# Performance work log

Hardware: AMD Instinct MI355X
Metric: run time of the kernel (lower is better)

## Reference

```python
import jax, jax.numpy as jnp
import numpy as np

K, N, D, M, M_RF, N_RF = 512, 512, 16, 64, 16, 64


def cmul(a, b):
    # complex matmul with stacked real/imag in axis -3: a [...,2,m,k], b [...,2,k,n]
    ar, ai = a[..., 0, :, :], a[..., 1, :, :]
    br, bi = b[..., 0, :, :], b[..., 1, :, :]
    return jnp.stack([ar @ br - ai @ bi, ar @ bi + ai @ br], axis=-3)


def conjT(a):
    # complex conjugate transpose
    ar, ai = a[..., 0, :, :], a[..., 1, :, :]
    return jnp.stack([jnp.swapaxes(ar, -1, -2), -jnp.swapaxes(ai, -1, -2)], axis=-3)


def cinv(a):
    # inverse of complex matrix a=[2,n,n] via real 2n x 2n block matrix
    ar, ai = a[0], a[1]
    n = ar.shape[0]
    Mblk = jnp.block([[ar, -ai], [ai, ar]])
    Minv = jnp.linalg.inv(Mblk)
    return jnp.stack([Minv[:n, :n], Minv[n:, :n]], axis=0)


def setup_inputs() -> dict:
    key = jax.random.key(0)
    ks = jax.random.split(key, 8)
    s = 0.05  # keep accumulated products well-scaled
    H = s * jax.random.normal(ks[0], (K, 2, M, N), jnp.float32)
    U_RF = s * jax.random.normal(ks[1], (K, 2, M, M_RF), jnp.float32)
    U_BB = s * jax.random.normal(ks[2], (K, 2, M_RF, D), jnp.float32)
    W = s * jax.random.normal(ks[3], (K, 2, D, D), jnp.float32)
    V_RF = s * jax.random.normal(ks[4], (2, N, N_RF), jnp.float32)
    V_BB = s * jax.random.normal(ks[5], (K, 2, N_RF, D), jnp.float32)
    Y = s * jax.random.normal(ks[6], (K, 2, N, D), jnp.float32)
    rho = jnp.ones((1,), jnp.float32)  # forward arg, unused by the module
    rho_X_layer = jnp.asarray(6.0, jnp.float32)  # learned scalar
    mu = jnp.asarray(1.0, jnp.float32)           # learned scalar
    params4 = 0.001 * jax.random.normal(ks[7], (K, 2, N, D), jnp.float32)
    return dict(H=H, U_RF=U_RF, U_BB=U_BB, W=W, V_RF=V_RF, V_BB=V_BB, Y=Y,
                rho=rho, rho_X_layer=rho_X_layer, mu=mu, params4=params4)


def reference(H, U_RF, U_BB, W, V_RF, V_BB, Y, rho, rho_X_layer, mu, params4):
    # temp[k] = H[k]^H U_RF[k] U_BB[k] : [K,2,N,d]
    temp = cmul(cmul(conjT(H), U_RF), U_BB)
    TW = cmul(temp, W)  # [K,2,N,d]
    # A_rho = sum_k temp W temp^H + I/(2 rho) : [2,N,N]
    A_rho = cmul(TW, conjT(temp)).sum(axis=0)
    I = jnp.stack([jnp.eye(N, dtype=H.dtype), jnp.zeros((N, N), H.dtype)], axis=0)
    A_rho = A_rho + (1.0 / (2.0 * rho_X_layer)) * I
    # B_rho[k] = temp W + 0.5*(V_RF V_BB[k]/rho - Y[k]) : [K,2,N,d]
    B_rho = TW + 0.5 * ((1.0 / rho_X_layer) * cmul(V_RF, V_BB) - Y)
    A_inv = cinv(A_rho + mu * I)  # [2,N,N]
    X = cmul(A_inv, B_rho) + params4  # [K,2,N,d]
    return X
```

## Files before the change

### kernel.cpp

```cpp
#include <hip/hip_runtime.h>

#define KK 512
#define NN 512
#define DD 16
#define MM 64
#define MRF 16
#define NRF 64

typedef __attribute__((ext_vector_type(8))) short bf16x8;
typedef __attribute__((ext_vector_type(4))) float f32x4;
typedef __attribute__((ext_vector_type(8))) unsigned short u16x8;
typedef __attribute__((ext_vector_type(4))) unsigned short u16x4;

#define MFMA16 __builtin_amdgcn_mfma_f32_16x16x32_bf16

static __device__ __forceinline__ unsigned short f2bf(float x) {
    unsigned int u = __float_as_uint(x);
    u += 0x7fffu + ((u >> 16) & 1u);
    return (unsigned short)(u >> 16);
}
static __device__ __forceinline__ float bf2f(unsigned short b) {
    return __uint_as_float((unsigned int)b << 16);
}
static __device__ __forceinline__ unsigned int pk2(float lo, float hi) {
    return (unsigned int)f2bf(lo) | ((unsigned int)f2bf(hi) << 16);
}

union frag_cast { uint4 u; bf16x8 v; };

__global__ __launch_bounds__(256) void vrfb_kernel(
    const float* __restrict__ V_RF, unsigned short* __restrict__ VRFb)
{
    const int idx = blockIdx.x*256 + threadIdx.x;
    const int n = idx >> 7, j = idx & 127;
    const int p = j >> 6, r = j & 63;
    VRFb[idx] = f2bf(V_RF[((size_t)p*NN + n)*NRF + r]);
}

__global__ __launch_bounds__(256) void small_kernel(
    const float* __restrict__ U_RF, const float* __restrict__ U_BB,
    const float* __restrict__ W, const float* __restrict__ V_BB,
    unsigned int* __restrict__ GT2f)
{
    const int k = blockIdx.x, t = threadIdx.x;
    __shared__ float sUR[2][MM][17];
    __shared__ float sUB[2][MRF][DD], sW[2][DD][DD];
    __shared__ float sVB[2][NRF][17];
    __shared__ float sG[2][MM][17], sGW[2][MM][17];

    const float* uf = U_RF + (size_t)k*2*MM*MRF;
    for (int i = t; i < 2*MM*MRF; i += 256) sUR[i>>10][(i>>4)&63][i&15] = uf[i];
    const float* ub = U_BB + (size_t)k*2*MRF*DD;
    for (int i = t; i < 2*MRF*DD; i += 256) sUB[i>>8][(i>>4)&15][i&15] = ub[i];
    const float* ww = W + (size_t)k*2*DD*DD;
    for (int i = t; i < 2*DD*DD; i += 256) sW[i>>8][(i>>4)&15][i&15] = ww[i];
    const float* vb = V_BB + (size_t)k*2*NRF*DD;
    for (int i = t; i < 2*NRF*DD; i += 256) sVB[i>>10][(i>>4)&63][i&15] = vb[i];
    __syncthreads();

    {
        const int m = t >> 2, dq = (t & 3) * 4;
        float gr[4] = {0,0,0,0}, gi[4] = {0,0,0,0};
#pragma unroll
        for (int r = 0; r < MRF; ++r) {
            const float ur = sUR[0][m][r], ui = sUR[1][m][r];
#pragma unroll
            for (int q = 0; q < 4; ++q) {
                const float br = sUB[0][r][dq+q], bi = sUB[1][r][dq+q];
                gr[q] += ur*br - ui*bi;
                gi[q] += ur*bi + ui*br;
            }
        }
#pragma unroll
        for (int q = 0; q < 4; ++q) { sG[0][m][dq+q] = gr[q]; sG[1][m][dq+q] = gi[q]; }
    }
    __syncthreads();

    {
        const int m = t >> 2, dq = (t & 3) * 4;
        float gwr[4] = {0,0,0,0}, gwi[4] = {0,0,0,0};
#pragma unroll
        for (int dp = 0; dp < DD; ++dp) {
            const float gr = sG[0][m][dp], gi = sG[1][m][dp];
#pragma unroll
            for (int q = 0; q < 4; ++q) {
                const float wr = sW[0][dp][dq+q], wi = sW[1][dp][dq+q];
                gwr[q] += gr*wr - gi*wi;
                gwi[q] += gr*wi + gi*wr;
            }
        }
#pragma unroll
        for (int q = 0; q < 4; ++q) { sGW[0][m][dq+q] = gwr[q]; sGW[1][m][dq+q] = gwi[q]; }
    }
    __syncthreads();

    {
        const int lane64 = t & 63, ks = t >> 6;
        const int c = lane64 & 15, kg = lane64 >> 4;
        const int e2b = ks*16 + kg*4;
        unsigned int* dstk = GT2f + (size_t)k*6144 + ks*1536 + lane64*4;
#pragma unroll
        for (int s = 0; s < 6; ++s) {
            uint4 o;
#pragma unroll
            for (int j = 0; j < 4; ++j) {
                const int e2 = e2b + j;
                const int sl0 = 2*e2;
                const int m0 = sl0 & 63, hi = sl0 >> 6;
                const int m1 = m0 + 1;
                float v0, v1;
                if (s == 0)      { v0 = hi ? sG[1][m0][c]   : sG[0][m0][c];
                                   v1 = hi ? sG[1][m1][c]   : sG[0][m1][c]; }
                else if (s == 1) { v0 = hi ? -sG[0][m0][c]  : sG[1][m0][c];
                                   v1 = hi ? -sG[0][m1][c]  : sG[1][m1][c]; }
                else if (s == 2) { v0 = hi ? sGW[1][m0][c]  : sGW[0][m0][c];
                                   v1 = hi ? sGW[1][m1][c]  : sGW[0][m1][c]; }
                else if (s == 3) { v0 = hi ? -sGW[0][m0][c] : sGW[1][m0][c];
                                   v1 = hi ? -sGW[0][m1][c] : sGW[1][m1][c]; }
                else if (s == 4) { v0 = hi ? -sVB[1][m0][c] : sVB[0][m0][c];
                                   v1 = hi ? -sVB[1][m1][c] : sVB[0][m1][c]; }
                else             { v0 = hi ? sVB[0][m0][c]  : sVB[1][m0][c];
                                   v1 = hi ? sVB[0][m1][c]  : sVB[1][m1][c]; }
                ((unsigned int*)&o)[j] = pk2(v0, v1);
            }
            *reinterpret_cast<uint4*>(dstk + s*256) = o;
        }
    }
}

__global__ __launch_bounds__(512, 8) void prep_main(
    const float* __restrict__ H, const unsigned int* __restrict__ GT2f,
    const unsigned short* __restrict__ VRFb,
    const float* __restrict__ Y, const float* __restrict__ rhoX,
    unsigned short* __restrict__ tempb, unsigned short* __restrict__ TWb,
    unsigned short* __restrict__ Bb)
{
    const int nb = blockIdx.x & 3;
    const int k  = blockIdx.x >> 2;
    const int t  = threadIdx.x;
    const int n0 = nb*128;

    __shared__ unsigned int sH[64][129];

    const float* Hk = H + (size_t)k*128*NN + n0;
#pragma unroll
    for (int pass = 0; pass < 4; ++pass) {
        const int e2 = pass*16 + (t >> 5);
        const int c4 = (t & 31) * 4;
        const float4 a = *reinterpret_cast<const float4*>(Hk + (size_t)(2*e2  )*NN + c4);
        const float4 b = *reinterpret_cast<const float4*>(Hk + (size_t)(2*e2+1)*NN + c4);
        uint4 d;
        d.x = pk2(a.x, b.x); d.y = pk2(a.y, b.y);
        d.z = pk2(a.z, b.z); d.w = pk2(a.w, b.w);
        *reinterpret_cast<uint4*>(&sH[e2][c4]) = d;
    }

    const int w = t >> 6, lane = t & 63;
    const int c = lane & 15, kg = lane >> 4;
    const float irx = 1.f / rhoX[0];
    const int ncol = w*16 + c;
    const int n = n0 + ncol;

    const size_t o0 = ((size_t)(k*2 + 0)*NN + n)*DD + kg*4;
    const size_t o1 = ((size_t)(k*2 + 1)*NN + n)*DD + kg*4;
    const float4 y0 = *reinterpret_cast<const float4*>(Y + o0);
    const float4 y1 = *reinterpret_cast<const float4*>(Y + o1);

    __syncthreads();

    f32x4 aTr = (f32x4)0.f, aTi = (f32x4)0.f;
    f32x4 aWr = (f32x4)0.f, aWi = (f32x4)0.f;
    f32x4 aVr = (f32x4)0.f, aVi = (f32x4)0.f;

    const unsigned int* gk = GT2f + (size_t)k*6144 + lane*4;

#pragma unroll
    for (int ks = 0; ks < 4; ++ks) {
        const int slot0 = ks*32 + kg*8;
        const int e2b = ks*16 + kg*4;
        frag_cast fh, g0, g1, g2, g3, v0, v1;
        fh.u.x = sH[e2b+0][ncol];
        fh.u.y = sH[e2b+1][ncol];
        fh.u.z = sH[e2b+2][ncol];
        fh.u.w = sH[e2b+3][ncol];
        const unsigned int* gb = gk + ks*1536;
        g0.u = *reinterpret_cast<const uint4*>(gb);
        g1.u = *reinterpret_cast<const uint4*>(gb + 256);
        g2.u = *reinterpret_cast<const uint4*>(gb + 512);
        g3.u = *reinterpret_cast<const uint4*>(gb + 768);
        v0.u = *reinterpret_cast<const uint4*>(gb + 1024);
        v1.u = *reinterpret_cast<const uint4*>(gb + 1280);
        const bf16x8 bv = *reinterpret_cast<const bf16x8*>(VRFb + (size_t)n*128 + slot0);

        aTr = MFMA16(g0.v, fh.v, aTr, 0, 0, 0);
        aTi = MFMA16(g1.v, fh.v, aTi, 0, 0, 0);
        aWr = MFMA16(g2.v, fh.v, aWr, 0, 0, 0);
        aWi = MFMA16(g3.v, fh.v, aWi, 0, 0, 0);
        aVr = MFMA16(v0.v, bv, aVr, 0, 0, 0);
        aVi = MFMA16(v1.v, bv, aVi, 0, 0, 0);
    }

    {
        const float y0a[4] = {y0.x, y0.y, y0.z, y0.w};
        const float y1a[4] = {y1.x, y1.y, y1.z, y1.w};
        u16x4 tr_, ti_, wr_, wi_, br_, bi_;
#pragma unroll
        for (int r = 0; r < 4; ++r) {
            tr_[r] = f2bf(aTr[r]);  ti_[r] = f2bf(aTi[r]);
            wr_[r] = f2bf(aWr[r]);  wi_[r] = f2bf(aWi[r]);
            br_[r] = f2bf(aWr[r] + 0.5f*(aVr[r]*irx - y0a[r]));
            bi_[r] = f2bf(aWi[r] + 0.5f*(aVi[r]*irx - y1a[r]));
        }
        *reinterpret_cast<u16x4*>(tempb + o0) = tr_;
        *reinterpret_cast<u16x4*>(tempb + o1) = ti_;
        *reinterpret_cast<u16x4*>(TWb + o0)   = wr_;
        *reinterpret_cast<u16x4*>(TWb + o1)   = wi_;
        *reinterpret_cast<u16x4*>(Bb + o0)    = br_;
        *reinterpret_cast<u16x4*>(Bb + o1)    = bi_;
    }
}

__global__ __launch_bounds__(256) void egemm_kernel(
    const unsigned short* __restrict__ TWb, const unsigned short* __restrict__ tmpb,
    float* __restrict__ Epart)
{
    const int ib = blockIdx.x >> 3;
    const int ks = blockIdx.x & 7;
    const int jb = blockIdx.y;
    const int w    = threadIdx.x >> 6;
    const int lane = threadIdx.x & 63;
    const int m  = lane & 15;
    const int kg = lane >> 4;
    const int iw = ib*64 + (w>>1)*32;
    const int jw = jb*64 + (w&1)*32;
    const int d0  = (kg & 1) * 8;
    const int kof = kg >> 1;

    f32x4 RR[2][2], II[2][2], RI[2][2], IR[2][2];
#pragma unroll
    for (int is = 0; is < 2; ++is)
#pragma unroll
        for (int js = 0; js < 2; ++js) {
            RR[is][js] = (f32x4)0.f; II[is][js] = (f32x4)0.f;
            RI[is][js] = (f32x4)0.f; IR[is][js] = (f32x4)0.f;
        }

#pragma unroll 2
    for (int c = 0; c < 32; ++c) {
        const int chunk = ks*32 + c;
        const int kp = chunk*2 + kof;
        const unsigned short* Ab = TWb  + ((size_t)(kp*2+0)*NN + iw + m)*DD + d0;
        const unsigned short* Bb2 = tmpb + ((size_t)(kp*2+0)*NN + jw + m)*DD + d0;
        bf16x8 ar[2], ai[2], br[2], bi[2];
#pragma unroll
        for (int is = 0; is < 2; ++is) {
            ar[is] = *reinterpret_cast<const bf16x8*>(Ab + (size_t)is*16*DD);
            ai[is] = *reinterpret_cast<const bf16x8*>(Ab + (size_t)NN*DD + (size_t)is*16*DD);
        }
#pragma unroll
        for (int js = 0; js < 2; ++js) {
            br[js] = *reinterpret_cast<const bf16x8*>(Bb2 + (size_t)js*16*DD);
            bi[js] = *reinterpret_cast<const bf16x8*>(Bb2 + (size_t)NN*DD + (size_t)js*16*DD);
        }
#pragma unroll
        for (int is = 0; is < 2; ++is)
#pragma unroll
            for (int js = 0; js < 2; ++js) {
                RR[is][js] = MFMA16(ar[is], br[js], RR[is][js], 0, 0, 0);
                II[is][js] = MFMA16(ai[is], bi[js], II[is][js], 0, 0, 0);
                RI[is][js] = MFMA16(ar[is], bi[js], RI[is][js], 0, 0, 0);
                IR[is][js] = MFMA16(ai[is], br[js], IR[is][js], 0, 0, 0);
            }
    }

    float* Eb = Epart + (size_t)ks*2*NN*NN;
#pragma unroll
    for (int is = 0; is < 2; ++is)
#pragma unroll
        for (int js = 0; js < 2; ++js) {
            const int i = iw + is*16 + kg*4;
            const int jx = jw + js*16 + m;
#pragma unroll
            for (int r = 0; r < 4; ++r) {
                Eb[(size_t)(i+r)*NN + jx]               = RR[is][js][r] + II[is][js][r];
                Eb[(size_t)NN*NN + (size_t)(i+r)*NN + jx] = IR[is][js][r] - RI[is][js][r];
            }
        }
}

__global__ __launch_bounds__(256) void reduceinit_kernel(
    const float* __restrict__ Epart,
    const float* __restrict__ rhoX, const float* __restrict__ mu,
    unsigned short* __restrict__ P, unsigned short* __restrict__ PT,
    unsigned short* __restrict__ T1, unsigned short* __restrict__ T1T)
{
    const size_t idx = (size_t)blockIdx.x*256 + threadIdx.x;
    const float ic = 1.f / (1.f/(2.f*rhoX[0]) + mu[0]);
    const size_t pl = (size_t)2*NN*NN;
    float s = 0.f;
#pragma unroll
    for (int ks = 0; ks < 8; ++ks) s += Epart[(size_t)ks*pl + idx];
    const float mm = s * ic;
    const int p = (int)(idx / ((size_t)NN*NN));
    const size_t rem = idx - (size_t)p*NN*NN;
    const int i = (int)(rem / NN), jx = (int)(rem % NN);
    const unsigned short pv = f2bf(-mm);
    const unsigned short tv = f2bf(((p == 0 && i == jx) ? 1.f : 0.f) - mm);
    const size_t tidx = (size_t)p*NN*NN + (size_t)jx*NN + i;
    P[idx] = pv;  PT[tidx] = pv;
    T1[idx] = tv; T1T[tidx] = tv;
}

template<bool ADD_B, bool WRITE_T>
__global__ __launch_bounds__(256) void mm_kernel(
    const unsigned short* __restrict__ A, const unsigned short* __restrict__ BT,
    unsigned short* __restrict__ D, unsigned short* __restrict__ DT)
{
    const int w    = threadIdx.x >> 6;
    const int lane = threadIdx.x & 63;
    const int m  = lane & 15;
    const int kg = lane >> 4;
    const int i0 = blockIdx.y*32;
    const int j0 = blockIdx.x*32;
    const int iw = (w>>1)*16;
    const int jw = (w&1)*16;

    __shared__ unsigned short sD[2][32][34];

    f32x4 RR = (f32x4)0.f, II = (f32x4)0.f, RI = (f32x4)0.f, IR = (f32x4)0.f;

#pragma unroll 8
    for (int c = 0; c < 16; ++c) {
        const int l0 = c*32 + kg*8;
        const bf16x8 ar = *reinterpret_cast<const bf16x8*>(A  + (size_t)(i0+iw+m)*NN + l0);
        const bf16x8 ai = *reinterpret_cast<const bf16x8*>(A  + (size_t)NN*NN + (size_t)(i0+iw+m)*NN + l0);
        const bf16x8 br = *reinterpret_cast<const bf16x8*>(BT + (size_t)(j0+jw+m)*NN + l0);
        const bf16x8 bi = *reinterpret_cast<const bf16x8*>(BT + (size_t)NN*NN + (size_t)(j0+jw+m)*NN + l0);
        RR = MFMA16(ar, br, RR, 0, 0, 0);
        II = MFMA16(ai, bi, II, 0, 0, 0);
        RI = MFMA16(ar, bi, RI, 0, 0, 0);
        IR = MFMA16(ai, br, IR, 0, 0, 0);
    }
    const int i = i0 + iw + kg*4;
    const int jx = j0 + jw + m;
    float adr[4] = {0.f,0.f,0.f,0.f}, adi[4] = {0.f,0.f,0.f,0.f};
    if (ADD_B) {
        const u16x4 badr = *reinterpret_cast<const u16x4*>(BT + (size_t)jx*NN + i);
        const u16x4 badi = *reinterpret_cast<const u16x4*>(BT + (size_t)NN*NN + (size_t)jx*NN + i);
#pragma unroll
        for (int r = 0; r < 4; ++r) { adr[r] = bf2f(badr[r]); adi[r] = bf2f(badi[r]); }
    }
#pragma unroll
    for (int r = 0; r < 4; ++r) {
        const unsigned short dr_ = f2bf(RR[r] - II[r] + adr[r]);
        const unsigned short di_ = f2bf(RI[r] + IR[r] + adi[r]);
        D[(size_t)(i+r)*NN + jx] = dr_;
        D[(size_t)NN*NN + (size_t)(i+r)*NN + jx] = di_;
        if (WRITE_T) {
            sD[0][iw + kg*4 + r][jw + m] = dr_;
            sD[1][iw + kg*4 + r][jw + m] = di_;
        }
    }
    if (WRITE_T) {
        __syncthreads();
        const int t = threadIdx.x;
        const int r8 = t >> 2, seg = t & 3;
        const int plane = r8 >> 5, jloc = r8 & 31;
        u16x8 v;
#pragma unroll
        for (int e = 0; e < 8; ++e) v[e] = sD[plane][seg*8 + e][jloc];
        *reinterpret_cast<u16x8*>(DT + (size_t)plane*NN*NN +
                                  (size_t)(j0 + jloc)*NN + i0 + seg*8) = v;
    }
}

__global__ __launch_bounds__(256) void final_kernel(
    const unsigned short* __restrict__ Sb, const unsigned short* __restrict__ Bb,
    const float* __restrict__ par4,
    const float* __restrict__ rhoX, const float* __restrict__ mu,
    float* __restrict__ Xout)
{
    const int k0 = blockIdx.x * 2;
    __shared__ __align__(16) unsigned short sBT[2][2][DD][520];

#pragma unroll
    for (int kk = 0; kk < 2; ++kk) {
        const unsigned short* Bk = Bb + (size_t)(k0 + kk)*2*NN*DD;
        for (int q = 0; q < 8; ++q) {
            const int t8 = q*256 + threadIdx.x;
            const u16x8 v = *reinterpret_cast<const u16x8*>(Bk + (size_t)t8*8);
            const int flat = t8*8;
            const int p = flat >> 13, n = (flat >> 4) & 511, dd0 = flat & 15;
#pragma unroll
            for (int jj = 0; jj < 8; ++jj) sBT[kk][p][dd0+jj][n] = v[jj];
        }
    }
    __syncthreads();

    const int w    = threadIdx.x >> 6;
    const int lane = threadIdx.x & 63;
    const int m  = lane & 15;
    const int kg = lane >> 4;
    const int i0 = blockIdx.y*64 + w*16;

    f32x4 RR[2], II[2], RI[2], IR[2];
#pragma unroll
    for (int kk = 0; kk < 2; ++kk) {
        RR[kk] = (f32x4)0.f; II[kk] = (f32x4)0.f;
        RI[kk] = (f32x4)0.f; IR[kk] = (f32x4)0.f;
    }

#pragma unroll 2
    for (int c = 0; c < 16; ++c) {
        const int l0 = c*32 + kg*8;
        const bf16x8 ar = *reinterpret_cast<const bf16x8*>(Sb + (size_t)(i0+m)*NN + l0);
        const bf16x8 ai = *reinterpret_cast<const bf16x8*>(Sb + (size_t)NN*NN + (size_t)(i0+m)*NN + l0);
#pragma unroll
        for (int kk = 0; kk < 2; ++kk) {
            const bf16x8 br = *reinterpret_cast<const bf16x8*>(&sBT[kk][0][m][l0]);
            const bf16x8 bi = *reinterpret_cast<const bf16x8*>(&sBT[kk][1][m][l0]);
            RR[kk] = MFMA16(ar, br, RR[kk], 0, 0, 0);
            II[kk] = MFMA16(ai, bi, II[kk], 0, 0, 0);
            RI[kk] = MFMA16(ar, bi, RI[kk], 0, 0, 0);
            IR[kk] = MFMA16(ai, br, IR[kk], 0, 0, 0);
        }
    }
    const float ic = 1.f / (1.f/(2.f*rhoX[0]) + mu[0]);
#pragma unroll
    for (int kk = 0; kk < 2; ++kk) {
        const int k = k0 + kk;
#pragma unroll
        for (int r = 0; r < 4; ++r) {
            const int i = i0 + kg*4 + r;
            const int d = m;
            const size_t idx0 = ((size_t)(k*2+0)*NN + i)*DD + d;
            const size_t idx1 = ((size_t)(k*2+1)*NN + i)*DD + d;
            Xout[idx0] = (RR[kk][r] - II[kk][r])*ic + par4[idx0];
            Xout[idx1] = (RI[kk][r] + IR[kk][r])*ic + par4[idx1];
        }
    }
}

extern "C" void kernel_launch(void* const* d_in, const int* in_sizes, int n_in,
                              void* d_out, int out_size, void* d_ws, size_t ws_size,
                              hipStream_t stream) {
    const float* H     = (const float*)d_in[0];
    const float* U_RF  = (const float*)d_in[1];
    const float* U_BB  = (const float*)d_in[2];
    const float* W     = (const float*)d_in[3];
    const float* V_RF  = (const float*)d_in[4];
    const float* V_BB  = (const float*)d_in[5];
    const float* Y     = (const float*)d_in[6];
    const float* rhoX  = (const float*)d_in[8];
    const float* mu    = (const float*)d_in[9];
    const float* par4  = (const float*)d_in[10];
    float* Xout = (float*)d_out;

    unsigned short* u = (unsigned short*)d_ws;
    const size_t bigE = (size_t)KK*2*NN*DD;
    const size_t plE  = (size_t)2*NN*NN;
    unsigned short* tempb = u;
    unsigned short* TWb   = tempb + bigE;
    unsigned short* Bb    = TWb + bigE;
    unsigned int*   GT2f  = (unsigned int*)(Bb + bigE);
    unsigned short* VRFb  = (unsigned short*)(GT2f + (size_t)KK*6144);
    unsigned short* Pm    = VRFb + (size_t)NN*128;
    unsigned short* PmT   = Pm  + plE;
    unsigned short* T1    = PmT + plE;
    unsigned short* T1T   = T1  + plE;
    unsigned short* Q     = T1T + plE;
    unsigned short* QT    = Q   + plE;
    unsigned short* R     = QT  + plE;
    unsigned short* RT    = R   + plE;
    unsigned short* T2    = RT  + plE;
    unsigned short* T2T   = T2  + plE;
    unsigned short* T3    = T2T + plE;
    unsigned short* T3T   = T3  + plE;
    unsigned short* R2    = T3T + plE;
    unsigned short* Ss    = R2  + plE;
    float* Epart = (float*)(Ss + plE);

    vrfb_kernel<<<256, 256, 0, stream>>>(V_RF, VRFb);
    small_kernel<<<KK, 256, 0, stream>>>(U_RF, U_BB, W, V_BB, GT2f);
    prep_main<<<KK*4, 512, 0, stream>>>(H, GT2f, VRFb, Y, rhoX,
                                        tempb, TWb, Bb);
    egemm_kernel<<<dim3(64, 8), 256, 0, stream>>>(TWb, tempb, Epart);
    reduceinit_kernel<<<(int)(plE/256), 256, 0, stream>>>(Epart, rhoX, mu,
                                                          Pm, PmT, T1, T1T);
    mm_kernel<false,true ><<<dim3(16,16), 256, 0, stream>>>(Pm, PmT, Q,  QT);
    mm_kernel<true ,true ><<<dim3(16,16), 256, 0, stream>>>(Q,  T1T, T2, T2T);
    mm_kernel<false,true ><<<dim3(16,16), 256, 0, stream>>>(Q,  QT,  R,  RT);
    mm_kernel<true ,true ><<<dim3(16,16), 256, 0, stream>>>(R,  T2T, T3, T3T);
    mm_kernel<false,false><<<dim3(16,16), 256, 0, stream>>>(R,  RT,  R2, nullptr);
    mm_kernel<true ,false><<<dim3(16,16), 256, 0, stream>>>(R2, T3T, Ss, nullptr);
    final_kernel<<<dim3(KK/2, 8), 256, 0, stream>>>(Ss, Bb, par4, rhoX, mu, Xout);
}
```

Before: 218.7 us.

## Fold V_RF conversion into small_kernel and widen prep_main tiles to 256 columns

```diff
diff --git a/kernel.cpp b/kernel.cpp
--- a/kernel.cpp
+++ b/kernel.cpp
@@ -28,25 +28,22 @@
 
 union frag_cast { uint4 u; bf16x8 v; };
 
-__global__ __launch_bounds__(256) void vrfb_kernel(
-    const float* __restrict__ V_RF, unsigned short* __restrict__ VRFb)
-{
-    const int idx = blockIdx.x*256 + threadIdx.x;
-    const int n = idx >> 7, j = idx & 127;
-    const int p = j >> 6, r = j & 63;
-    VRFb[idx] = f2bf(V_RF[((size_t)p*NN + n)*NRF + r]);
-}
-
 __global__ __launch_bounds__(256) void small_kernel(
     const float* __restrict__ U_RF, const float* __restrict__ U_BB,
     const float* __restrict__ W, const float* __restrict__ V_BB,
-    unsigned int* __restrict__ GT2f)
+    const float* __restrict__ V_RF,
+    unsigned int* __restrict__ GT2f, unsigned short* __restrict__ VRFb)
 {
     const int k = blockIdx.x, t = threadIdx.x;
     __shared__ float sUR[2][MM][17];
     __shared__ float sUB[2][MRF][DD], sW[2][DD][DD];
     __shared__ float sVB[2][NRF][17];
     __shared__ float sG[2][MM][17], sGW[2][MM][17];
+
+    if (t < 128) {
+        const int p = t >> 6, r = t & 63;
+        VRFb[(size_t)k*128 + t] = f2bf(V_RF[((size_t)p*NN + k)*NRF + r]);
+    }
 
     const float* uf = U_RF + (size_t)k*2*MM*MRF;
     for (int i = t; i < 2*MM*MRF; i += 256) sUR[i>>10][(i>>4)&63][i&15] = uf[i];
@@ -128,25 +125,25 @@
     }
 }
 
-__global__ __launch_bounds__(512, 8) void prep_main(
+__global__ __launch_bounds__(512, 4) void prep_main(
     const float* __restrict__ H, const unsigned int* __restrict__ GT2f,
     const unsigned short* __restrict__ VRFb,
     const float* __restrict__ Y, const float* __restrict__ rhoX,
     unsigned short* __restrict__ tempb, unsigned short* __restrict__ TWb,
     unsigned short* __restrict__ Bb)
 {
-    const int nb = blockIdx.x & 3;
-    const int k  = blockIdx.x >> 2;
+    const int nb = blockIdx.x & 1;
+    const int k  = blockIdx.x >> 1;
     const int t  = threadIdx.x;
-    const int n0 = nb*128;
-
-    __shared__ unsigned int sH[64][129];
+    const int n0 = nb*256;
+
+    __shared__ unsigned int sH[64][260];
 
     const float* Hk = H + (size_t)k*128*NN + n0;
 #pragma unroll
-    for (int pass = 0; pass < 4; ++pass) {
-        const int e2 = pass*16 + (t >> 5);
-        const int c4 = (t & 31) * 4;
+    for (int pass = 0; pass < 8; ++pass) {
+        const int e2 = pass*8 + (t >> 6);
+        const int c4 = (t & 63) * 4;
         const float4 a = *reinterpret_cast<const float4*>(Hk + (size_t)(2*e2  )*NN + c4);
         const float4 b = *reinterpret_cast<const float4*>(Hk + (size_t)(2*e2+1)*NN + c4);
         uint4 d;
@@ -158,19 +155,26 @@
     const int w = t >> 6, lane = t & 63;
     const int c = lane & 15, kg = lane >> 4;
     const float irx = 1.f / rhoX[0];
-    const int ncol = w*16 + c;
-    const int n = n0 + ncol;
-
-    const size_t o0 = ((size_t)(k*2 + 0)*NN + n)*DD + kg*4;
-    const size_t o1 = ((size_t)(k*2 + 1)*NN + n)*DD + kg*4;
-    const float4 y0 = *reinterpret_cast<const float4*>(Y + o0);
-    const float4 y1 = *reinterpret_cast<const float4*>(Y + o1);
+    const int ncolA = w*16 + c;
+    const int ncolB = ncolA + 128;
+    const int nA = n0 + ncolA;
+    const int nB = n0 + ncolB;
+
+    const size_t oA0 = ((size_t)(k*2 + 0)*NN + nA)*DD + kg*4;
+    const size_t oA1 = ((size_t)(k*2 + 1)*NN + nA)*DD + kg*4;
+    const size_t oB0 = ((size_t)(k*2 + 0)*NN + nB)*DD + kg*4;
+    const size_t oB1 = ((size_t)(k*2 + 1)*NN + nB)*DD + kg*4;
+    const float4 yA0 = *reinterpret_cast<const float4*>(Y + oA0);
+    const float4 yA1 = *reinterpret_cast<const float4*>(Y + oA1);
+    const float4 yB0 = *reinterpret_cast<const float4*>(Y + oB0);
+    const float4 yB1 = *reinterpret_cast<const float4*>(Y + oB1);
 
     __syncthreads();
 
-    f32x4 aTr = (f32x4)0.f, aTi = (f32x4)0.f;
-    f32x4 aWr = (f32x4)0.f, aWi = (f32x4)0.f;
-    f32x4 aVr = (f32x4)0.f, aVi = (f32x4)0.f;
+    f32x4 aTrA = (f32x4)0.f, aTiA = (f32x4)0.f, aWrA = (f32x4)0.f,
+          aWiA = (f32x4)0.f, aVrA = (f32x4)0.f, aViA = (f32x4)0.f;
+    f32x4 aTrB = (f32x4)0.f, aTiB = (f32x4)0.f, aWrB = (f32x4)0.f,
+          aWiB = (f32x4)0.f, aVrB = (f32x4)0.f, aViB = (f32x4)0.f;
 
     const unsigned int* gk = GT2f + (size_t)k*6144 + lane*4;
 
@@ -178,11 +182,15 @@
     for (int ks = 0; ks < 4; ++ks) {
         const int slot0 = ks*32 + kg*8;
         const int e2b = ks*16 + kg*4;
-        frag_cast fh, g0, g1, g2, g3, v0, v1;
-        fh.u.x = sH[e2b+0][ncol];
-        fh.u.y = sH[e2b+1][ncol];
-        fh.u.z = sH[e2b+2][ncol];
-        fh.u.w = sH[e2b+3][ncol];
+        frag_cast fhA, fhB, g0, g1, g2, g3, v0, v1;
+        fhA.u.x = sH[e2b+0][ncolA];
+        fhA.u.y = sH[e2b+1][ncolA];
+        fhA.u.z = sH[e2b+2][ncolA];
+        fhA.u.w = sH[e2b+3][ncolA];
+        fhB.u.x = sH[e2b+0][ncolB];
+        fhB.u.y = sH[e2b+1][ncolB];
+        fhB.u.z = sH[e2b+2][ncolB];
+        fhB.u.w = sH[e2b+3][ncolB];
         const unsigned int* gb = gk + ks*1536;
         g0.u = *reinterpret_cast<const uint4*>(gb);
         g1.u = *reinterpret_cast<const uint4*>(gb + 256);
@@ -190,33 +198,58 @@
         g3.u = *reinterpret_cast<const uint4*>(gb + 768);
         v0.u = *reinterpret_cast<const uint4*>(gb + 1024);
         v1.u = *reinterpret_cast<const uint4*>(gb + 1280);
-        const bf16x8 bv = *reinterpret_cast<const bf16x8*>(VRFb + (size_t)n*128 + slot0);
-
-        aTr = MFMA16(g0.v, fh.v, aTr, 0, 0, 0);
-        aTi = MFMA16(g1.v, fh.v, aTi, 0, 0, 0);
-        aWr = MFMA16(g2.v, fh.v, aWr, 0, 0, 0);
-        aWi = MFMA16(g3.v, fh.v, aWi, 0, 0, 0);
-        aVr = MFMA16(v0.v, bv, aVr, 0, 0, 0);
-        aVi = MFMA16(v1.v, bv, aVi, 0, 0, 0);
+        const bf16x8 bvA = *reinterpret_cast<const bf16x8*>(VRFb + (size_t)nA*128 + slot0);
+        const bf16x8 bvB = *reinterpret_cast<const bf16x8*>(VRFb + (size_t)nB*128 + slot0);
+
+        aTrA = MFMA16(g0.v, fhA.v, aTrA, 0, 0, 0);
+        aTrB = MFMA16(g0.v, fhB.v, aTrB, 0, 0, 0);
+        aTiA = MFMA16(g1.v, fhA.v, aTiA, 0, 0, 0);
+        aTiB = MFMA16(g1.v, fhB.v, aTiB, 0, 0, 0);
+        aWrA = MFMA16(g2.v, fhA.v, aWrA, 0, 0, 0);
+        aWrB = MFMA16(g2.v, fhB.v, aWrB, 0, 0, 0);
+        aWiA = MFMA16(g3.v, fhA.v, aWiA, 0, 0, 0);
+        aWiB = MFMA16(g3.v, fhB.v, aWiB, 0, 0, 0);
+        aVrA = MFMA16(v0.v, bvA, aVrA, 0, 0, 0);
+        aVrB = MFMA16(v0.v, bvB, aVrB, 0, 0, 0);
+        aViA = MFMA16(v1.v, bvA, aViA, 0, 0, 0);
+        aViB = MFMA16(v1.v, bvB, aViB, 0, 0, 0);
     }
 
     {
-        const float y0a[4] = {y0.x, y0.y, y0.z, y0.w};
-        const float y1a[4] = {y1.x, y1.y, y1.z, y1.w};
+        const float y0a[4] = {yA0.x, yA0.y, yA0.z, yA0.w};
+        const float y1a[4] = {yA1.x, yA1.y, yA1.z, yA1.w};
         u16x4 tr_, ti_, wr_, wi_, br_, bi_;
 #pragma unroll
         for (int r = 0; r < 4; ++r) {
-            tr_[r] = f2bf(aTr[r]);  ti_[r] = f2bf(aTi[r]);
-            wr_[r] = f2bf(aWr[r]);  wi_[r] = f2bf(aWi[r]);
-            br_[r] = f2bf(aWr[r] + 0.5f*(aVr[r]*irx - y0a[r]));
-            bi_[r] = f2bf(aWi[r] + 0.5f*(aVi[r]*irx - y1a[r]));
-        }
-        *reinterpret_cast<u16x4*>(tempb + o0) = tr_;
-        *reinterpret_cast<u16x4*>(tempb + o1) = ti_;
-        *reinterpret_cast<u16x4*>(TWb + o0)   = wr_;
-        *reinterpret_cast<u16x4*>(TWb + o1)   = wi_;
-        *reinterpret_cast<u16x4*>(Bb + o0)    = br_;
-        *reinterpret_cast<u16x4*>(Bb + o1)    = bi_;
+            tr_[r] = f2bf(aTrA[r]);  ti_[r] = f2bf(aTiA[r]);
+            wr_[r] = f2bf(aWrA[r]);  wi_[r] = f2bf(aWiA[r]);
+            br_[r] = f2bf(aWrA[r] + 0.5f*(aVrA[r]*irx - y0a[r]));
+            bi_[r] = f2bf(aWiA[r] + 0.5f*(aViA[r]*irx - y1a[r]));
+        }
+        *reinterpret_cast<u16x4*>(tempb + oA0) = tr_;
+        *reinterpret_cast<u16x4*>(tempb + oA1) = ti_;
+        *reinterpret_cast<u16x4*>(TWb + oA0)   = wr_;
+        *reinterpret_cast<u16x4*>(TWb + oA1)   = wi_;
+        *reinterpret_cast<u16x4*>(Bb + oA0)    = br_;
+        *reinterpret_cast<u16x4*>(Bb + oA1)    = bi_;
+    }
+    {
+        const float y0a[4] = {yB0.x, yB0.y, yB0.z, yB0.w};
+        const float y1a[4] = {yB1.x, yB1.y, yB1.z, yB1.w};
+        u16x4 tr_, ti_, wr_, wi_, br_, bi_;
+#pragma unroll
+        for (int r = 0; r < 4; ++r) {
+            tr_[r] = f2bf(aTrB[r]);  ti_[r] = f2bf(aTiB[r]);
+            wr_[r] = f2bf(aWrB[r]);  wi_[r] = f2bf(aWiB[r]);
+            br_[r] = f2bf(aWrB[r] + 0.5f*(aVrB[r]*irx - y0a[r]));
+            bi_[r] = f2bf(aWiB[r] + 0.5f*(aViB[r]*irx - y1a[r]));
+        }
+        *reinterpret_cast<u16x4*>(tempb + oB0) = tr_;
+        *reinterpret_cast<u16x4*>(tempb + oB1) = ti_;
+        *reinterpret_cast<u16x4*>(TWb + oB0)   = wr_;
+        *reinterpret_cast<u16x4*>(TWb + oB1)   = wi_;
+        *reinterpret_cast<u16x4*>(Bb + oB0)    = br_;
+        *reinterpret_cast<u16x4*>(Bb + oB1)    = bi_;
     }
 }
 
@@ -245,7 +278,7 @@
             RI[is][js] = (f32x4)0.f; IR[is][js] = (f32x4)0.f;
         }
 
-#pragma unroll 2
+#pragma unroll 4
     for (int c = 0; c < 32; ++c) {
         const int chunk = ks*32 + c;
         const int kp = chunk*2 + kof;
@@ -410,7 +443,7 @@
         RI[kk] = (f32x4)0.f; IR[kk] = (f32x4)0.f;
     }
 
-#pragma unroll 2
+#pragma unroll 4
     for (int c = 0; c < 16; ++c) {
         const int l0 = c*32 + kg*8;
         const bf16x8 ar = *reinterpret_cast<const bf16x8*>(Sb + (size_t)(i0+m)*NN + l0);
@@ -480,9 +513,8 @@
     unsigned short* Ss    = R2  + plE;
     float* Epart = (float*)(Ss + plE);
 
-    vrfb_kernel<<<256, 256, 0, stream>>>(V_RF, VRFb);
-    small_kernel<<<KK, 256, 0, stream>>>(U_RF, U_BB, W, V_BB, GT2f);
-    prep_main<<<KK*4, 512, 0, stream>>>(H, GT2f, VRFb, Y, rhoX,
+    small_kernel<<<KK, 256, 0, stream>>>(U_RF, U_BB, W, V_BB, V_RF, GT2f, VRFb);
+    prep_main<<<KK*2, 512, 0, stream>>>(H, GT2f, VRFb, Y, rhoX,
                                         tempb, TWb, Bb);
     egemm_kernel<<<dim3(64, 8), 256, 0, stream>>>(TWb, tempb, Epart);
     reduceinit_kernel<<<(int)(plE/256), 256, 0, stream>>>(Epart, rhoX, mu,
```

Result: slower. 234.2 us (+7.1%).
